# Kernel optimization log

Hardware: AMD Instinct MI355X
Metric: run time of the kernel (lower is better)

The kernel has to match this reference:

```python
import jax, jax.numpy as jnp
import numpy as np

VOCAB, EMBED, HIDDEN, NUM_OUT = 50000, 256, 64, 16
BATCH, T = 64, 2048
BN_EPS = 1e-5


def setup_inputs() -> dict:
    key = jax.random.key(0)
    ks = jax.random.split(key, 12)
    x = jax.random.randint(ks[0], (BATCH, T), 0, VOCAB, dtype=jnp.int64)
    seq_lengths = jax.random.randint(ks[1], (BATCH,), 1, T, dtype=jnp.int64)
    emb = jax.random.normal(ks[2], (VOCAB, EMBED), dtype=jnp.float32) * 0.1
    emb = emb.at[0].set(0.0)  # padding_idx=0
    s_ih = 1.0 / np.sqrt(HIDDEN)
    W_ih = jax.random.uniform(ks[3], (4 * HIDDEN, EMBED), jnp.float32, -s_ih, s_ih)
    W_hh = jax.random.uniform(ks[4], (4 * HIDDEN, HIDDEN), jnp.float32, -s_ih, s_ih)
    b_ih = jax.random.uniform(ks[5], (4 * HIDDEN,), jnp.float32, -s_ih, s_ih)
    b_hh = jax.random.uniform(ks[6], (4 * HIDDEN,), jnp.float32, -s_ih, s_ih)
    bn_gamma = jnp.ones((HIDDEN,), jnp.float32)
    bn_beta = jnp.zeros((HIDDEN,), jnp.float32)
    bn_mean = jnp.zeros((HIDDEN,), jnp.float32)
    bn_var = jnp.ones((HIDDEN,), jnp.float32)
    s_fc = 1.0 / np.sqrt(HIDDEN)
    fc_w = jax.random.uniform(ks[7], (NUM_OUT, HIDDEN), jnp.float32, -s_fc, s_fc)
    fc_b = jax.random.uniform(ks[8], (NUM_OUT,), jnp.float32, -s_fc, s_fc)
    return {"x": x, "seq_lengths": seq_lengths, "emb": emb, "W_ih": W_ih,
            "W_hh": W_hh, "b_ih": b_ih, "b_hh": b_hh, "bn_gamma": bn_gamma,
            "bn_beta": bn_beta, "bn_mean": bn_mean, "bn_var": bn_var,
            "fc_w": fc_w, "fc_b": fc_b}


def reference(x, seq_lengths, emb, W_ih, W_hh, b_ih, b_hh,
              bn_gamma, bn_beta, bn_mean, bn_var, fc_w, fc_b):
    B, Tn = x.shape
    H = W_hh.shape[1]
    x_embed = emb[x]                       # [B, T, E] (dropout is identity in eval)
    xe_t = jnp.transpose(x_embed, (1, 0, 2))  # [T, B, E] time-major for scan
    # precompute input projections for all timesteps in one big GEMM
    gx = jnp.einsum('tbe,ge->tbg', xe_t, W_ih) + b_ih + b_hh  # [T, B, 4H]

    def step(carry, gxt):
        h, c = carry
        gates = gxt + h @ W_hh.T           # [B, 4H]
        i, f, g, o = jnp.split(gates, 4, axis=-1)  # torch LSTMCell gate order
        i = jax.nn.sigmoid(i)
        f = jax.nn.sigmoid(f)
        g = jnp.tanh(g)
        o = jax.nn.sigmoid(o)
        c = f * c + i * g
        h = o * jnp.tanh(c)
        return (h, c), None

    h0 = jnp.zeros((B, H), x_embed.dtype)
    c0 = jnp.zeros((B, H), x_embed.dtype)
    (h_last, _), _ = jax.lax.scan(step, (h0, c0), gx)
    # BatchNorm1d (eval mode: running stats)
    h_bn = (h_last - bn_mean) * jax.lax.rsqrt(bn_var + BN_EPS) * bn_gamma + bn_beta
    return h_bn @ fc_w.T + fc_b            # [B, num_output]
```

## Files before the change

kernel.cpp:

```cpp
#include <hip/hip_runtime.h>
#include <math.h>

#define VOCAB   50000
#define EMBED   256
#define HIDDEN  64
#define G4      256
#define BATCH   64
#define TSEQ    2048
#define NUM_OUT 16

typedef _Float16 h2   __attribute__((ext_vector_type(2)));
typedef _Float16 f16x8 __attribute__((ext_vector_type(8)));
typedef float    f32x4 __attribute__((ext_vector_type(4)));

#define LOG2E  1.4426950408889634f
#define LOG2E2 2.8853900817779268f

__device__ __forceinline__ float fexp2f(float x) { return __builtin_amdgcn_exp2f(x); }
__device__ __forceinline__ float frcpf(float x)  { return __builtin_amdgcn_rcpf(x); }

__device__ __forceinline__ float dot2(h2 a, h2 b, float c) {
#if __has_builtin(__builtin_amdgcn_fdot2)
    return __builtin_amdgcn_fdot2(a, b, c, false);
#else
    float r;
    asm("v_dot2_f32_f16 %0, %1, %2, %3"
        : "=v"(r)
        : "v"(__builtin_bit_cast(int, a)), "v"(__builtin_bit_cast(int, b)), "v"(c));
    return r;
#endif
}

template <int CTRL>
__device__ __forceinline__ float dppf(float v) {
    return __int_as_float(__builtin_amdgcn_update_dpp(
        0, __float_as_int(v), CTRL, 0xF, 0xF, true));
}

#define REP32(M) M(0) M(1) M(2) M(3) M(4) M(5) M(6) M(7) \
                 M(8) M(9) M(10) M(11) M(12) M(13) M(14) M(15) \
                 M(16) M(17) M(18) M(19) M(20) M(21) M(22) M(23) \
                 M(24) M(25) M(26) M(27) M(28) M(29) M(30) M(31)

__global__ __launch_bounds__(256) void proj_mfma(
    const float* __restrict__ emb, const float* __restrict__ W_ih,
    const float* __restrict__ b_ih, const float* __restrict__ b_hh,
    float* __restrict__ proj)
{
    const int tid  = threadIdx.x;
    const int w    = tid >> 6;
    const int lane = tid & 63;
    const int R0   = blockIdx.x * 64;

    const int rowA  = R0 + w * 16 + (lane & 15);
    const int rowAc = rowA < VOCAB ? rowA : VOCAB - 1;
    const int kb    = (lane >> 4) * 8;
    const float* arow = emb + (size_t)rowAc * EMBED + kb;

    f32x4 acc[16];
    #pragma unroll
    for (int t = 0; t < 16; ++t) acc[t] = f32x4{0.f, 0.f, 0.f, 0.f};

    #pragma unroll
    for (int kc = 0; kc < 8; ++kc) {
        float4 alo = *(const float4*)(arow + kc * 32);
        float4 ahi = *(const float4*)(arow + kc * 32 + 4);
        f16x8 af;
        af[0] = (_Float16)alo.x; af[1] = (_Float16)alo.y;
        af[2] = (_Float16)alo.z; af[3] = (_Float16)alo.w;
        af[4] = (_Float16)ahi.x; af[5] = (_Float16)ahi.y;
        af[6] = (_Float16)ahi.z; af[7] = (_Float16)ahi.w;
        #pragma unroll
        for (int t = 0; t < 16; ++t) {
            const float* brow = W_ih + (size_t)(t * 16 + (lane & 15)) * EMBED
                                + kc * 32 + kb;
            float4 blo = *(const float4*)brow;
            float4 bhi = *(const float4*)(brow + 4);
            f16x8 bf;
            bf[0] = (_Float16)blo.x; bf[1] = (_Float16)blo.y;
            bf[2] = (_Float16)blo.z; bf[3] = (_Float16)blo.w;
            bf[4] = (_Float16)bhi.x; bf[5] = (_Float16)bhi.y;
            bf[6] = (_Float16)bhi.z; bf[7] = (_Float16)bhi.w;
            acc[t] = __builtin_amdgcn_mfma_f32_16x16x32_f16(af, bf, acc[t], 0, 0, 0);
        }
    }

    const int crow0 = R0 + w * 16 + (lane >> 4) * 4;
    const int colin = lane & 15;
    #pragma unroll
    for (int t = 0; t < 16; ++t) {
        int g = t * 16 + colin;
        float bias = b_ih[g] + b_hh[g];
        float sc = ((g >> 6) == 2) ? LOG2E2 : LOG2E;
        #pragma unroll
        for (int j = 0; j < 4; ++j) {
            int row = crow0 + j;
            if (row < VOCAB)
                proj[(size_t)row * G4 + g] = (acc[t][j] + bias) * sc;
        }
    }
}

__global__ __launch_bounds__(256) void lstm_scan(
    const int* __restrict__ x, const float* __restrict__ proj,
    const float* __restrict__ W_hh,
    const float* __restrict__ bn_gamma, const float* __restrict__ bn_beta,
    const float* __restrict__ bn_mean, const float* __restrict__ bn_var,
    const float* __restrict__ fc_w, const float* __restrict__ fc_b,
    float* __restrict__ out)
{
    const int b   = blockIdx.x;
    const int tid = threadIdx.x;
    const int w   = tid >> 6;
    const int l   = tid & 63;
    const int q   = l & 3;
    const int unit = w * 16 + (l >> 2);

    __shared__ int   toks[TSEQ + 8];
    __shared__ __align__(16) short hbuf[2][HIDDEN];
    __shared__ float hfin[HIDDEN];
    __shared__ float hb_s[HIDDEN];

    for (int i = tid; i < TSEQ + 8; i += 256)
        toks[i] = x[b * TSEQ + (i < TSEQ ? i : TSEQ - 1)];
    if (tid < 2 * HIDDEN) ((short*)hbuf)[tid] = 0;

    const float s_k = (q == 2) ? LOG2E2 : LOG2E;
    const float* Wr = &W_hh[(size_t)(q * HIDDEN + unit) * HIDDEN];
#define WR_DECL(n) h2 wr##n;
    REP32(WR_DECL)
#undef WR_DECL
#define WR_LOAD(n) { float2 v = *(const float2*)&Wr[2 * (n)]; \
                     wr##n = h2{(_Float16)(v.x * s_k), (_Float16)(v.y * s_k)}; }
    REP32(WR_LOAD)
#undef WR_LOAD

    const float s_c = (q == 2) ? LOG2E2 : 1.0f;
    const float s_m = (q == 2) ? 2.0f * LOG2E2 : 1.0f;
    const bool qodd = (q & 1) != 0;
    const bool qhi  = (q & 2) != 0;

    float c = 0.0f, hmy = 0.0f;
    const float* projw = proj + q * HIDDEN + unit;

    __syncthreads();

    float gx0 = projw[(size_t)toks[0] * G4];
    float gx1 = projw[(size_t)toks[1] * G4];
    float gx2 = projw[(size_t)toks[2] * G4];
    float gx3 = projw[(size_t)toks[3] * G4];
    int tk0 = toks[4], tk1 = toks[5], tk2 = toks[6], tk3 = toks[7];

    const int4* hp0 = (const int4*)hbuf[0];
    const int4* hp1 = (const int4*)hbuf[1];

#define DOTG(R, W0, W1, W2, W3) \
    a0 = dot2(W0, __builtin_bit_cast(h2, R.x), a0); \
    a1 = dot2(W1, __builtin_bit_cast(h2, R.y), a1); \
    a2 = dot2(W2, __builtin_bit_cast(h2, R.z), a2); \
    a3 = dot2(W3, __builtin_bit_cast(h2, R.w), a3);

#define STEP(HP, WB, GX, TK, TT) { \
    int4 r0 = (HP)[0], r1 = (HP)[1], r2 = (HP)[2], r3 = (HP)[3]; \
    int4 r4 = (HP)[4], r5 = (HP)[5], r6 = (HP)[6], r7 = (HP)[7]; \
    int tnew = toks[(TT) + 8]; \
    float gnew = projw[(size_t)(TK) * G4]; \
    float a0 = GX, a1 = 0.f, a2 = 0.f, a3 = 0.f; \
    DOTG(r0, wr0,  wr1,  wr2,  wr3)  DOTG(r1, wr4,  wr5,  wr6,  wr7) \
    DOTG(r2, wr8,  wr9,  wr10, wr11) DOTG(r3, wr12, wr13, wr14, wr15) \
    DOTG(r4, wr16, wr17, wr18, wr19) DOTG(r5, wr20, wr21, wr22, wr23) \
    DOTG(r6, wr24, wr25, wr26, wr27) DOTG(r7, wr28, wr29, wr30, wr31) \
    float gv = (a0 + a1) + (a2 + a3); \
    GX = gnew; TK = tnew; \
    float tt2 = fexp2f(gv); \
    float rr = fmaf(-s_m, frcpf(tt2 + 1.0f), s_c);        \
    float b1 = dppf<0xB1>(rr);                            \
    float b2 = dppf<0x4E>(rr);                            \
    float b3 = dppf<0x1B>(rr);                            \
    float A  = qodd ? b1 : rr,  B  = qodd ? b3 : b2; \
    float A2 = qodd ? rr : b1,  B2 = qodd ? b2 : b3; \
    float i_ = qhi ? B  : A,    g_ = qhi ? A  : B; \
    float f_ = qhi ? B2 : A2,   o_ = qhi ? A2 : B2; \
    float o2 = o_ + o_; \
    c = fmaf(f_, c, i_ * g_);                             \
    float e2 = fexp2f(c); \
    float rv = frcpf(e2 + 1.0f); \
    hmy = fmaf(-o2, rv, o_);                              \
    if (q == 0) hbuf[WB][unit] = __builtin_bit_cast(short, (_Float16)hmy); \
    asm volatile("s_waitcnt lgkmcnt(0)" ::: "memory"); \
    __builtin_amdgcn_s_barrier(); \
    asm volatile("" ::: "memory"); \
}

    for (int t = 0; t < TSEQ; t += 4) {
        STEP(hp0, 1, gx0, tk0, t)
        STEP(hp1, 0, gx1, tk1, t + 1)
        STEP(hp0, 1, gx2, tk2, t + 2)
        STEP(hp1, 0, gx3, tk3, t + 3)
    }
#undef STEP
#undef DOTG

    if (q == 0) hfin[unit] = hmy;
    __syncthreads();
    if (tid < HIDDEN) {
        float hb = (hfin[tid] - bn_mean[tid]) * rsqrtf(bn_var[tid] + 1e-5f)
                   * bn_gamma[tid] + bn_beta[tid];
        hb_s[tid] = hb;
    }
    __syncthreads();
    if (tid < NUM_OUT) {
        float s0 = fc_b[tid], s1 = 0.f, s2 = 0.f, s3 = 0.f;
        #pragma unroll
        for (int k = 0; k < HIDDEN; k += 4) {
            s0 = fmaf(hb_s[k + 0], fc_w[tid * HIDDEN + k + 0], s0);
            s1 = fmaf(hb_s[k + 1], fc_w[tid * HIDDEN + k + 1], s1);
            s2 = fmaf(hb_s[k + 2], fc_w[tid * HIDDEN + k + 2], s2);
            s3 = fmaf(hb_s[k + 3], fc_w[tid * HIDDEN + k + 3], s3);
        }
        out[b * NUM_OUT + tid] = (s0 + s1) + (s2 + s3);
    }
}

extern "C" void kernel_launch(void* const* d_in, const int* in_sizes, int n_in,
                              void* d_out, int out_size, void* d_ws, size_t ws_size,
                              hipStream_t stream) {
    const int*   x        = (const int*)d_in[0];
    const float* emb      = (const float*)d_in[2];
    const float* W_ih     = (const float*)d_in[3];
    const float* W_hh     = (const float*)d_in[4];
    const float* b_ih     = (const float*)d_in[5];
    const float* b_hh     = (const float*)d_in[6];
    const float* bn_gamma = (const float*)d_in[7];
    const float* bn_beta  = (const float*)d_in[8];
    const float* bn_mean  = (const float*)d_in[9];
    const float* bn_var   = (const float*)d_in[10];
    const float* fc_w     = (const float*)d_in[11];
    const float* fc_b     = (const float*)d_in[12];

    float* proj = (float*)d_ws;

    proj_mfma<<<(VOCAB + 63) / 64, 256, 0, stream>>>(emb, W_ih, b_ih, b_hh, proj);

    lstm_scan<<<BATCH, 256, 0, stream>>>(x, proj, W_hh,
                                         bn_gamma, bn_beta, bn_mean, bn_var,
                                         fc_w, fc_b, (float*)d_out);
}
```

Baseline: 715.4 us.

## Pre-convert W_ih to fp16 and stage embedding tile in LDS for projection GEMM

Adds a small kernel that converts W_ih to fp16 once into a device global buffer, so the projection GEMM loads B fragments as fp16 vectors instead of reloading and converting fp32 per tile. The embedding tile is loaded coalesced, converted to fp16 and staged in padded shared memory before the MFMA loop. This targets global traffic and conversion ALU work in the projection kernel. The cost is an extra kernel launch, a barrier, and shared memory use that may lower occupancy; the dominant cost is likely the sequential LSTM scan, which is unchanged.

```diff
diff --git a/kernel.cpp b/kernel.cpp
--- a/kernel.cpp
+++ b/kernel.cpp
@@ -9,7 +9,7 @@
 #define TSEQ    2048
 #define NUM_OUT 16
 
-typedef _Float16 h2   __attribute__((ext_vector_type(2)));
+typedef _Float16 h2    __attribute__((ext_vector_type(2)));
 typedef _Float16 f16x8 __attribute__((ext_vector_type(8)));
 typedef float    f32x4 __attribute__((ext_vector_type(4)));
 
@@ -42,45 +42,60 @@
                  M(16) M(17) M(18) M(19) M(20) M(21) M(22) M(23) \
                  M(24) M(25) M(26) M(27) M(28) M(29) M(30) M(31)
 
+__device__ __align__(16) short g_Wf16[G4 * EMBED];
+
+__global__ __launch_bounds__(256) void wcvt_kernel(const float* __restrict__ W_ih) {
+    int i = (blockIdx.x * 256 + threadIdx.x) * 4;
+    float4 v = *(const float4*)&W_ih[i];
+    short4 o;
+    o.x = __builtin_bit_cast(short, (_Float16)v.x);
+    o.y = __builtin_bit_cast(short, (_Float16)v.y);
+    o.z = __builtin_bit_cast(short, (_Float16)v.z);
+    o.w = __builtin_bit_cast(short, (_Float16)v.w);
+    *(short4*)&g_Wf16[i] = o;
+}
+
 __global__ __launch_bounds__(256) void proj_mfma(
-    const float* __restrict__ emb, const float* __restrict__ W_ih,
+    const float* __restrict__ emb,
     const float* __restrict__ b_ih, const float* __restrict__ b_hh,
     float* __restrict__ proj)
 {
+    __shared__ __align__(16) short As[64][264];
+
     const int tid  = threadIdx.x;
     const int w    = tid >> 6;
     const int lane = tid & 63;
     const int R0   = blockIdx.x * 64;
 
-    const int rowA  = R0 + w * 16 + (lane & 15);
-    const int rowAc = rowA < VOCAB ? rowA : VOCAB - 1;
-    const int kb    = (lane >> 4) * 8;
-    const float* arow = emb + (size_t)rowAc * EMBED + kb;
+    #pragma unroll
+    for (int it = 0; it < 16; ++it) {
+        int flat = it * 256 + tid;
+        int r  = flat >> 6;
+        int c4 = flat & 63;
+        int row = R0 + r; row = row < VOCAB ? row : VOCAB - 1;
+        float4 v = *(const float4*)&emb[(size_t)row * EMBED + c4 * 4];
+        short4 o;
+        o.x = __builtin_bit_cast(short, (_Float16)v.x);
+        o.y = __builtin_bit_cast(short, (_Float16)v.y);
+        o.z = __builtin_bit_cast(short, (_Float16)v.z);
+        o.w = __builtin_bit_cast(short, (_Float16)v.w);
+        *(short4*)&As[r][c4 * 4] = o;
+    }
+    __syncthreads();
 
     f32x4 acc[16];
     #pragma unroll
     for (int t = 0; t < 16; ++t) acc[t] = f32x4{0.f, 0.f, 0.f, 0.f};
 
+    const short* arow = &As[w * 16 + (lane & 15)][(lane >> 4) * 8];
+    const int boff = (lane & 15) * EMBED + (lane >> 4) * 8;
+
     #pragma unroll
     for (int kc = 0; kc < 8; ++kc) {
-        float4 alo = *(const float4*)(arow + kc * 32);
-        float4 ahi = *(const float4*)(arow + kc * 32 + 4);
-        f16x8 af;
-        af[0] = (_Float16)alo.x; af[1] = (_Float16)alo.y;
-        af[2] = (_Float16)alo.z; af[3] = (_Float16)alo.w;
-        af[4] = (_Float16)ahi.x; af[5] = (_Float16)ahi.y;
-        af[6] = (_Float16)ahi.z; af[7] = (_Float16)ahi.w;
+        f16x8 af = *(const f16x8*)(arow + kc * 32);
         #pragma unroll
         for (int t = 0; t < 16; ++t) {
-            const float* brow = W_ih + (size_t)(t * 16 + (lane & 15)) * EMBED
-                                + kc * 32 + kb;
-            float4 blo = *(const float4*)brow;
-            float4 bhi = *(const float4*)(brow + 4);
-            f16x8 bf;
-            bf[0] = (_Float16)blo.x; bf[1] = (_Float16)blo.y;
-            bf[2] = (_Float16)blo.z; bf[3] = (_Float16)blo.w;
-            bf[4] = (_Float16)bhi.x; bf[5] = (_Float16)bhi.y;
-            bf[6] = (_Float16)bhi.z; bf[7] = (_Float16)bhi.w;
+            f16x8 bf = *(const f16x8*)&g_Wf16[t * 16 * EMBED + kc * 32 + boff];
             acc[t] = __builtin_amdgcn_mfma_f32_16x16x32_f16(af, bf, acc[t], 0, 0, 0);
         }
     }
@@ -240,7 +255,8 @@
 
     float* proj = (float*)d_ws;
 
-    proj_mfma<<<(VOCAB + 63) / 64, 256, 0, stream>>>(emb, W_ih, b_ih, b_hh, proj);
+    wcvt_kernel<<<G4 * EMBED / (256 * 4), 256, 0, stream>>>(W_ih);
+    proj_mfma<<<(VOCAB + 63) / 64, 256, 0, stream>>>(emb, b_ih, b_hh, proj);
 
     lstm_scan<<<BATCH, 256, 0, stream>>>(x, proj, W_hh,
                                          bn_gamma, bn_beta, bn_mean, bn_var,
```

New measurement: 642.6 us. 1.11x faster.
